# Performance work log

Hardware: AMD Instinct MI355X
Metric: run time of the kernel (lower is better)

## Reference

```python
import jax, jax.numpy as jnp
import numpy as np

ROPE_BASE = 10000.0
NEG_INF = -1e9


def _rope_tables(L, dh, dtype):
    # standard RoPE: inv_freq over half dims, tables shaped [L, dh]
    half = dh // 2
    inv_freq = 1.0 / (ROPE_BASE ** (jnp.arange(0, half, dtype=jnp.float32) * 2.0 / dh))
    freqs = jnp.arange(L, dtype=jnp.float32)[:, None] * inv_freq[None, :]  # [L, half]
    emb = jnp.concatenate([freqs, freqs], axis=-1)  # [L, dh]
    return jnp.cos(emb).astype(dtype), jnp.sin(emb).astype(dtype)


def _apply_rope(t, cos, sin):
    # t: [B, H, L, dh]; rotate-half convention
    dh = t.shape[-1]
    t1, t2 = t[..., : dh // 2], t[..., dh // 2:]
    rot = jnp.concatenate([-t2, t1], axis=-1)
    return t * cos[None, None] + rot * sin[None, None]


def setup_inputs() -> dict:
    key = jax.random.key(0)
    ks = jax.random.split(key, 7)
    B, L, D, nh = 2, 2048, 2048, 16
    s = 0.02
    return {
        "x": jax.random.normal(ks[0], (B, L, D), dtype=jnp.float32),
        "Wq": jax.random.normal(ks[1], (D, 2 * D), dtype=jnp.float32) * s,
        "Wk": jax.random.normal(ks[2], (D, D), dtype=jnp.float32) * s,
        "Wv": jax.random.normal(ks[3], (D, D), dtype=jnp.float32) * s,
        "Wl": jax.random.normal(ks[4], (D, nh), dtype=jnp.float32) * s,
        "bl": jnp.zeros((nh,), dtype=jnp.float32),
        "Wo": jax.random.normal(ks[5], (D, D), dtype=jnp.float32) * s,
    }


def reference(x, Wq, Wk, Wv, Wl, bl, Wo):
    B, L, D = x.shape
    nh = Wl.shape[1]
    dh = D // nh

    q = (x @ Wq).reshape(B, L, 2 * nh, dh).transpose(0, 2, 1, 3)  # [B, 2nh, L, dh]
    k = (x @ Wk).reshape(B, L, nh, dh).transpose(0, 2, 1, 3)      # [B, nh, L, dh]
    v = (x @ Wv).reshape(B, L, nh, dh).transpose(0, 2, 1, 3)      # [B, nh, L, dh]

    cos, sin = _rope_tables(L, dh, x.dtype)
    q = _apply_rope(q, cos, sin)
    k = _apply_rope(k, cos, sin)

    # pair query heads (2i, 2i+1) share k/v head i — avoid repeat_interleave
    qp = q.reshape(B, nh, 2, L, dh)
    scale = 1.0 / jnp.sqrt(jnp.asarray(dh, dtype=x.dtype))
    scores = jnp.einsum("bhpqd,bhkd->bhpqk", qp, k) * scale  # [B, nh, 2, L, L]
    causal = jnp.tril(jnp.ones((L, L), dtype=bool))
    scores = jnp.where(causal[None, None, None], scores, NEG_INF)
    probs = jax.nn.softmax(scores, axis=-1)
    ctx = jnp.einsum("bhpqk,bhkd->bhpqd", probs, v)  # [B, nh, 2, L, dh]

    lam = jax.nn.sigmoid(x @ Wl + bl).transpose(0, 2, 1)[..., None]  # [B, nh, L, 1]
    out = ctx[:, :, 0] - lam * ctx[:, :, 1]  # [B, nh, L, dh]
    out = out.transpose(0, 2, 1, 3).reshape(B, L, D)
    return out @ Wo
```

## Files before the change

### kernel.cpp

```cpp
#include <hip/hip_runtime.h>
#include <cstddef>
#include <cstdint>

#define L_SEQ 2048
#define D_MODEL 2048
#define NH 16
#define DH 128
#define M_ROWS 4096

__device__ __forceinline__ ushort f2bf(float f) {
    union { __bf16 b; ushort u; } v; v.b = (__bf16)f; return v.u;
}
__device__ __forceinline__ float bf2f(ushort h) {
    union { uint32_t u; float f; } v; v.u = ((uint32_t)h) << 16; return v.f;
}
__device__ __forceinline__ float2 bf2f2(uint32_t u) {
    union { uint32_t u; float f; } lo, hi;
    lo.u = u << 16; hi.u = u & 0xffff0000u;
    return make_float2(lo.f, hi.f);
}

__device__ __forceinline__ void gld_lds16(const void* g, void* l) {
    __builtin_amdgcn_global_load_lds(
        (const __attribute__((address_space(1))) void*)g,
        (__attribute__((address_space(3))) void*)l, 16, 0, 0);
}

typedef __bf16  bf16x8 __attribute__((ext_vector_type(8)));
typedef float   f32x4  __attribute__((ext_vector_type(4)));

__global__ __launch_bounds__(256) void cvt_bf16(
    const float* __restrict__ in, ushort* __restrict__ out)
{
    const int i = (blockIdx.x * 256 + threadIdx.x) * 8;
    const float4 a = *(const float4*)&in[i];
    const float4 b = *(const float4*)&in[i + 4];
    uint4 o;
    o.x = (uint)f2bf(a.x) | ((uint)f2bf(a.y) << 16);
    o.y = (uint)f2bf(a.z) | ((uint)f2bf(a.w) << 16);
    o.z = (uint)f2bf(b.x) | ((uint)f2bf(b.y) << 16);
    o.w = (uint)f2bf(b.z) | ((uint)f2bf(b.w) << 16);
    *(uint4*)&out[i] = o;
}

__global__ __launch_bounds__(256) void transpose_cvt(
    const float* __restrict__ W, ushort* __restrict__ Wt, int K, int N)
{
    __shared__ float tile[32][33];
    const int n0 = blockIdx.x * 32, k0 = blockIdx.y * 32;
    const int t = threadIdx.x;
    const int r = t >> 3;
    const int c4 = (t & 7) * 4;
    const float4 v = *(const float4*)&W[(size_t)(k0 + r) * N + n0 + c4];
    tile[r][c4 + 0] = v.x; tile[r][c4 + 1] = v.y;
    tile[r][c4 + 2] = v.z; tile[r][c4 + 3] = v.w;
    __syncthreads();
    ushort4 o;
    o.x = f2bf(tile[c4 + 0][r]);
    o.y = f2bf(tile[c4 + 1][r]);
    o.z = f2bf(tile[c4 + 2][r]);
    o.w = f2bf(tile[c4 + 3][r]);
    *(ushort4*)&Wt[(size_t)(n0 + r) * K + k0 + c4] = o;
}

__global__ __launch_bounds__(256) void rope_table(float2* __restrict__ tab)
{
    const int i = blockIdx.x * 256 + threadIdx.x;
    const int d = i & 63, l = i >> 6;
    const float inv = exp2f(-(float)d * 0.20762050593045857f);
    const float ang = (float)l * inv;
    float s, c;
    sincosf(ang, &s, &c);
    tab[i] = make_float2(c, s);
}

__global__ __launch_bounds__(256) void rope_k(
    ushort* __restrict__ T, const float2* __restrict__ tab)
{
    const int idx = blockIdx.x * 256 + threadIdx.x;
    const int d2   = (idx & 31) * 2;
    const int head = (idx >> 5) & 15;
    const int row  = idx >> 9;
    const int l    = row & (L_SEQ - 1);
    const size_t base = (size_t)row * 2048 + head * 128 + d2;
    const uint a = *(const uint*)&T[base];
    const uint b = *(const uint*)&T[base + 64];
    const float2 t0 = bf2f2(a);
    const float2 t1 = bf2f2(b);
    const float2 cs0 = tab[l * 64 + d2];
    const float2 cs1 = tab[l * 64 + d2 + 1];
    const float o0x = t0.x * cs0.x - t1.x * cs0.y;
    const float o0y = t0.y * cs1.x - t1.y * cs1.y;
    const float o1x = t1.x * cs0.x + t0.x * cs0.y;
    const float o1y = t1.y * cs1.x + t0.y * cs1.y;
    *(uint*)&T[base]      = (uint)f2bf(o0x) | ((uint)f2bf(o0y) << 16);
    *(uint*)&T[base + 64] = (uint)f2bf(o1x) | ((uint)f2bf(o1y) << 16);
}

template <int MODE>
__global__ __launch_bounds__(256) void gemm_bf16(
    const ushort* __restrict__ A, const ushort* __restrict__ Bt,
    void* __restrict__ Cv, int M, int N, int K)
{
    __shared__ __align__(16) ushort As[128 * 32];
    __shared__ __align__(16) ushort Bs[128 * 32];
    const int bm = blockIdx.y * 128;
    const int bn = blockIdx.x * 128;
    const int t = threadIdx.x;
    const int w = t >> 6, lane = t & 63;
    const int wm = (w & 1) * 64;
    const int wn = (w >> 1) * 64;

    const int srow = t >> 2;
    const int scol = (t & 3) * 8;
    const ushort* Ag  = A  + (size_t)(bm + srow) * K + scol;
    const ushort* Ag2 = A  + (size_t)(bm + 64 + srow) * K + scol;
    const ushort* Bg  = Bt + (size_t)(bn + srow) * K + scol;
    const ushort* Bg2 = Bt + (size_t)(bn + 64 + srow) * K + scol;
    ushort* Asl  = &As[(size_t)t * 8];
    ushort* Asl2 = &As[(size_t)(t + 256) * 8];
    ushort* Bsl  = &Bs[(size_t)t * 8];
    ushort* Bsl2 = &Bs[(size_t)(t + 256) * 8];

    const int fr = lane & 15;
    const int fq = (lane >> 4) * 8;
    const ushort* Abase = &As[(size_t)(wm + fr) * 32 + fq];
    const ushort* Bbase = &Bs[(size_t)(wn + fr) * 32 + fq];

    f32x4 acc[4][4] = {};

    for (int k0 = 0; k0 < K; k0 += 32) {
        __syncthreads();
        gld_lds16(Ag + k0, Asl);
        gld_lds16(Ag2 + k0, Asl2);
        gld_lds16(Bg + k0, Bsl);
        gld_lds16(Bg2 + k0, Bsl2);
        __syncthreads();
        bf16x8 a[4], b[4];
        #pragma unroll
        for (int i = 0; i < 4; ++i) {
            a[i] = *(const bf16x8*)(Abase + (size_t)i * 16 * 32);
            b[i] = *(const bf16x8*)(Bbase + (size_t)i * 16 * 32);
        }
        #pragma unroll
        for (int mt = 0; mt < 4; ++mt)
            #pragma unroll
            for (int nt = 0; nt < 4; ++nt)
                acc[mt][nt] = __builtin_amdgcn_mfma_f32_16x16x32_bf16(
                    a[mt], b[nt], acc[mt][nt], 0, 0, 0);
    }

    const int crow = (lane >> 4) * 4;
    const int ccol = lane & 15;
    #pragma unroll
    for (int mt = 0; mt < 4; ++mt) {
        #pragma unroll
        for (int nt = 0; nt < 4; ++nt) {
            if (MODE == 3) {
                const size_t row = bm + wm + mt * 16 + crow;
                const size_t col = bn + wn + nt * 16 + ccol;
                ushort4 o4;
                o4.x = f2bf(acc[mt][nt][0]); o4.y = f2bf(acc[mt][nt][1]);
                o4.z = f2bf(acc[mt][nt][2]); o4.w = f2bf(acc[mt][nt][3]);
                *(ushort4*)&((ushort*)Cv)[
                    ((row >> 11) * 16 + (col >> 7)) * (size_t)(128 * 2048)
                    + (col & 127) * 2048 + (row & 2047)] = o4;
            } else {
                #pragma unroll
                for (int reg = 0; reg < 4; ++reg) {
                    const size_t row = bm + wm + mt * 16 + crow + reg;
                    const size_t col = bn + wn + nt * 16 + ccol;
                    if (MODE == 1) {
                        ((ushort*)Cv)[row * N + col] = f2bf(acc[mt][nt][reg]);
                    } else {
                        ((float*)Cv)[row * N + col] = acc[mt][nt][reg];
                    }
                }
            }
        }
    }
}

__global__ __launch_bounds__(256) void lam_kernel(
    const float* __restrict__ X, const float* __restrict__ Wl,
    const float* __restrict__ bl, float* __restrict__ Lam)
{
    const int idx  = blockIdx.x * 256 + threadIdx.x;
    const int hh   = idx & 15;
    const int part = (idx >> 4) & 1;
    const int m    = idx >> 5;
    const float* xr = X + (size_t)m * D_MODEL + part * 1024;
    const float* wl = Wl + (size_t)(part * 1024) * NH;
    float acc = 0.0f;
    for (int d = 0; d < 1024; d += 4) {
        const float4 xv = *(const float4*)&xr[d];
        acc += xv.x * wl[(d + 0) * NH + hh];
        acc += xv.y * wl[(d + 1) * NH + hh];
        acc += xv.z * wl[(d + 2) * NH + hh];
        acc += xv.w * wl[(d + 3) * NH + hh];
    }
    acc += __shfl_xor(acc, 16);
    if (part == 0) {
        acc += bl[hh];
        Lam[(size_t)m * NH + hh] = 1.0f / (1.0f + expf(-acc));
    }
}

__global__ __launch_bounds__(256, 2) void attn_mfma(
    const ushort* __restrict__ Qb, const ushort* __restrict__ Kb,
    const ushort* __restrict__ Vtg, const float* __restrict__ Lam,
    const float2* __restrict__ Rtab, ushort* __restrict__ OutB)
{
    __shared__ __align__(16) ushort lds[33792];
    ushort* P_sh = lds + 24576;

    const int h  = blockIdx.y;
    const int b  = blockIdx.z;
    const int pt = blockIdx.x;
    const int t  = threadIdx.x;
    const int w = t >> 6, lane = t & 63;
    const int colL = lane & 15, quad = lane >> 4;
    const int p = w >> 1, slot = w & 1;
    ushort* Pw = P_sh + w * (32 * 72);

    const ushort* Kgbase = Kb  + (size_t)(b * 2048) * 2048 + h * 128;
    const ushort* Vgbase = Vtg + (size_t)((b * 16 + h) * 128) * 2048;
    const float scale2 = 0.12751744f;

    auto stageK = [&](ushort* dst, int kt0) {
        #pragma unroll
        for (int j = 0; j < 4; ++j) {
            const int idx = j * 256 + t;
            const int kr = idx >> 4;
            const int kg = t & 15;
            gld_lds16(Kgbase + (size_t)(kt0 + kr) * 2048 + ((kg ^ (kr & 15)) << 3),
                      dst + (size_t)idx * 8);
        }
    };
    auto stageV = [&](ushort* dst, int kt0) {
        #pragma unroll
        for (int j = 0; j < 4; ++j) {
            const int idx = j * 256 + t;
            const int vr = idx >> 3;
            const int vg = t & 7;
            gld_lds16(Vgbase + (size_t)vr * 2048 + kt0 + ((vg ^ (vr & 7)) << 3),
                      dst + (size_t)idx * 8);
        }
    };

    for (int ph = 0; ph < 2; ++ph) {
        const int qt  = ph ? pt : 31 - pt;
        const int q0  = qt * 64;
        const int r0w = q0 + slot * 32;

        bf16x8 qf[2][4];
        #pragma unroll
        for (int g = 0; g < 2; ++g) {
            const int l = r0w + g * 16 + colL;
            const ushort* Qr = Qb + (size_t)(b * 2048 + l) * 4096
                             + (2 * h + p) * 128 + quad * 8;
            ushort raw[4][8];
            #pragma unroll
            for (int c = 0; c < 4; ++c)
                *(uint4*)raw[c] = *(const uint4*)&Qr[c * 32];
            const float2* tb = Rtab + l * 64 + quad * 8;
            ushort o[4][8];
            #pragma unroll
            for (int c = 0; c < 2; ++c)
                #pragma unroll
                for (int j = 0; j < 8; ++j) {
                    const float2 cs = tb[c * 32 + j];
                    const float a  = bf2f(raw[c][j]);
                    const float bb = bf2f(raw[c + 2][j]);
                    o[c][j]     = f2bf(a * cs.x - bb * cs.y);
                    o[c + 2][j] = f2bf(bb * cs.x + a * cs.y);
                }
            #pragma unroll
            for (int c = 0; c < 4; ++c)
                qf[g][c] = *(const bf16x8*)o[c];
        }

        f32x4 ctx[2][8] = {};
        float m2[2][4] = {{-1e30f,-1e30f,-1e30f,-1e30f},
                          {-1e30f,-1e30f,-1e30f,-1e30f}};
        float li[2][4] = {};

        ushort* Kc = lds;
        ushort* Vc = lds + 8192;
        ushort* Fr = lds + 16384;

        stageK(Kc, 0);
        stageV(Vc, 0);
        __syncthreads();

        for (int kt = 0; kt <= qt; ++kt) {
            const int kt0 = kt * 64;

            f32x4 sc2[2][4] = {};
            __builtin_amdgcn_s_setprio(1);
            #pragma unroll
            for (int c = 0; c < 4; ++c)
                #pragma unroll
                for (int nt = 0; nt < 4; ++nt) {
                    const int krow = nt * 16 + colL;
                    const bf16x8 kf = *(const bf16x8*)
                        &Kc[krow * 128 + (((c * 4 + quad) ^ (krow & 15)) << 3)];
                    sc2[0][nt] = __builtin_amdgcn_mfma_f32_16x16x32_bf16(
                        qf[0][c], kf, sc2[0][nt], 0, 0, 0);
                    sc2[1][nt] = __builtin_amdgcn_mfma_f32_16x16x32_bf16(
                        qf[1][c], kf, sc2[1][nt], 0, 0, 0);
                }
            __builtin_amdgcn_s_setprio(0);

            __syncthreads();
            if (kt < qt) {
                stageK(Fr, kt0 + 64);
                stageV(Kc, kt0 + 64);
            }

            const bool dmask = (kt == qt);
            #pragma unroll
            for (int g = 0; g < 2; ++g)
                #pragma unroll
                for (int reg = 0; reg < 4; ++reg) {
                    const int row = r0w + g * 16 + quad * 4 + reg;
                    float s[4];
                    #pragma unroll
                    for (int nt = 0; nt < 4; ++nt) {
                        float v = sc2[g][nt][reg] * scale2;
                        if (dmask && (kt0 + nt * 16 + colL > row)) v = -1e9f;
                        s[nt] = v;
                    }
                    float mx = fmaxf(fmaxf(s[0], s[1]), fmaxf(s[2], s[3]));
                    #pragma unroll
                    for (int off = 8; off >= 1; off >>= 1)
                        mx = fmaxf(mx, __shfl_xor(mx, off));
                    if (__any(mx > m2[g][reg] + 11.0f)) {
                        const float mnew  = fmaxf(m2[g][reg], mx);
                        const float alpha = exp2f(m2[g][reg] - mnew);
                        li[g][reg] *= alpha;
                        m2[g][reg] = mnew;
                        #pragma unroll
                        for (int nt2 = 0; nt2 < 8; ++nt2)
                            ctx[g][nt2][reg] *= alpha;
                    }
                    float rs = 0.f;
                    #pragma unroll
                    for (int nt = 0; nt < 4; ++nt) {
                        const float pv = exp2f(s[nt] - m2[g][reg]);
                        s[nt] = pv;
                        rs += pv;
                    }
                    #pragma unroll
                    for (int off = 8; off >= 1; off >>= 1)
                        rs += __shfl_xor(rs, off);
                    li[g][reg] += rs;
                    #pragma unroll
                    for (int nt = 0; nt < 4; ++nt)
                        Pw[(g * 16 + quad * 4 + reg) * 72 + nt * 16 + colL]
                            = f2bf(s[nt]);
                }

            __builtin_amdgcn_s_setprio(1);
            #pragma unroll
            for (int c2 = 0; c2 < 2; ++c2) {
                const bf16x8 pf0 = *(const bf16x8*)
                    &Pw[colL * 72 + c2 * 32 + quad * 8];
                const bf16x8 pf1 = *(const bf16x8*)
                    &Pw[(16 + colL) * 72 + c2 * 32 + quad * 8];
                #pragma unroll
                for (int nt2 = 0; nt2 < 8; ++nt2) {
                    const int vrow = nt2 * 16 + colL;
                    const bf16x8 vf = *(const bf16x8*)
                        &Vc[vrow * 64 + (((c2 * 4 + quad) ^ (vrow & 7)) << 3)];
                    ctx[0][nt2] = __builtin_amdgcn_mfma_f32_16x16x32_bf16(
                        pf0, vf, ctx[0][nt2], 0, 0, 0);
                    ctx[1][nt2] = __builtin_amdgcn_mfma_f32_16x16x32_bf16(
                        pf1, vf, ctx[1][nt2], 0, 0, 0);
                }
            }
            __builtin_amdgcn_s_setprio(0);

            __syncthreads();
            ushort* tmp = Fr; Fr = Vc; Vc = Kc; Kc = tmp;
        }

        float invl[2][4];
        #pragma unroll
        for (int g = 0; g < 2; ++g)
            #pragma unroll
            for (int reg = 0; reg < 4; ++reg)
                invl[g][reg] = 1.0f / li[g][reg];

        float* comb = (float*)lds;
        __syncthreads();
        if (p == 1) {
            #pragma unroll
            for (int g = 0; g < 2; ++g)
                #pragma unroll
                for (int nt2 = 0; nt2 < 8; ++nt2)
                    #pragma unroll
                    for (int reg = 0; reg < 4; ++reg)
                        comb[(slot * 32 + g * 16 + quad * 4 + reg) * 130
                             + nt2 * 16 + colL] = ctx[g][nt2][reg] * invl[g][reg];
        }
        __syncthreads();
        if (p == 0) {
            #pragma unroll
            for (int g = 0; g < 2; ++g)
                #pragma unroll
                for (int reg = 0; reg < 4; ++reg) {
                    const int row = r0w + g * 16 + quad * 4 + reg;
                    const float lamv = Lam[(size_t)(b * 2048 + row) * 16 + h];
                    ushort* orow = OutB + (size_t)(b * 2048 + row) * 2048 + h * 128;
                    #pragma unroll
                    for (int nt2 = 0; nt2 < 8; ++nt2) {
                        const float c1 = comb[(slot * 32 + g * 16 + quad * 4 + reg) * 130
                                              + nt2 * 16 + colL];
                        const float o = ctx[g][nt2][reg] * invl[g][reg] - lamv * c1;
                        orow[nt2 * 16 + colL] = f2bf(o);
                    }
                }
        }
        __syncthreads();
    }
}

extern "C" void kernel_launch(void* const* d_in, const int* in_sizes, int n_in,
                              void* d_out, int out_size, void* d_ws, size_t ws_size,
                              hipStream_t stream)
{
    const float* x  = (const float*)d_in[0];
    const float* Wq = (const float*)d_in[1];
    const float* Wk = (const float*)d_in[2];
    const float* Wv = (const float*)d_in[3];
    const float* Wl = (const float*)d_in[4];
    const float* bl = (const float*)d_in[5];
    const float* Wo = (const float*)d_in[6];
    float* out = (float*)d_out;
    (void)ws_size; (void)in_sizes; (void)n_in; (void)out_size;

    ushort* ws   = (ushort*)d_ws;
    ushort* xb   = ws;
    ushort* Qb16 = xb   + (size_t)8388608;
    ushort* Kb16 = Qb16 + (size_t)16777216;
    ushort* Vtg  = Kb16 + (size_t)8388608;
    ushort* Wqt  = Vtg  + (size_t)8388608;
    ushort* Wkt  = Wqt  + (size_t)8388608;
    ushort* Wvt  = Wkt  + (size_t)4194304;
    ushort* Wot  = Wvt  + (size_t)4194304;
    ushort* OutB = Wot  + (size_t)4194304;
    float*  LamB = (float*)(OutB + (size_t)8388608);
    float2* Rtab = (float2*)(LamB + (size_t)65536);

    cvt_bf16<<<4096, 256, 0, stream>>>(x, xb);
    transpose_cvt<<<dim3(128, 64), 256, 0, stream>>>(Wq, Wqt, 2048, 4096);
    transpose_cvt<<<dim3(64, 64), 256, 0, stream>>>(Wk, Wkt, 2048, 2048);
    transpose_cvt<<<dim3(64, 64), 256, 0, stream>>>(Wv, Wvt, 2048, 2048);
    transpose_cvt<<<dim3(64, 64), 256, 0, stream>>>(Wo, Wot, 2048, 2048);
    lam_kernel<<<512, 256, 0, stream>>>(x, Wl, bl, LamB);
    rope_table<<<512, 256, 0, stream>>>(Rtab);

    gemm_bf16<1><<<dim3(32, 32), 256, 0, stream>>>(xb, Wqt, Qb16, M_ROWS, 4096, D_MODEL);
    gemm_bf16<1><<<dim3(16, 32), 256, 0, stream>>>(xb, Wkt, Kb16, M_ROWS, D_MODEL, D_MODEL);
    gemm_bf16<3><<<dim3(16, 32), 256, 0, stream>>>(xb, Wvt, Vtg, M_ROWS, D_MODEL, D_MODEL);

    rope_k<<<8192, 256, 0, stream>>>(Kb16, Rtab);

    attn_mfma<<<dim3(16, NH, 2), 256, 0, stream>>>(Qb16, Kb16, Vtg, LamB, Rtab, OutB);

    gemm_bf16<0><<<dim3(16, 32), 256, 0, stream>>>(OutB, Wot, out, M_ROWS, D_MODEL, D_MODEL);
}
```

Before: 632.7 us.

## Replace 128x128 GEMM with double-buffered 256x256 swizzled-LDS MFMA GEMM

The bf16 GEMM moves from 128x128 tiles with 4 waves and a single LDS buffer (BK=32) to 256x256 tiles with 8 waves, BK=64, XOR-swizzled LDS, and double buffering. The next K-tile is staged during MFMA compute, with interleaved barriers and setprio. The aim is more data reuse per byte loaded, hiding global load latency, and fewer LDS bank conflicts across all four projection GEMMs. In exchange it needs 128KB of LDS and many more accumulator registers per block. The grid also shrinks to 128–256 blocks, which may underfill the CUs.

Measured after the change: 649.0 us. 2.6% more time.

```diff
diff --git a/kernel.cpp b/kernel.cpp
--- a/kernel.cpp
+++ b/kernel.cpp
@@ -98,82 +98,123 @@
 }
 
 template <int MODE>
-__global__ __launch_bounds__(256) void gemm_bf16(
+__global__ __launch_bounds__(512, 2) void gemm256(
     const ushort* __restrict__ A, const ushort* __restrict__ Bt,
     void* __restrict__ Cv, int M, int N, int K)
 {
-    __shared__ __align__(16) ushort As[128 * 32];
-    __shared__ __align__(16) ushort Bs[128 * 32];
-    const int bm = blockIdx.y * 128;
-    const int bn = blockIdx.x * 128;
+    __shared__ __align__(16) ushort lds[65536];
     const int t = threadIdx.x;
-    const int w = t >> 6, lane = t & 63;
-    const int wm = (w & 1) * 64;
-    const int wn = (w >> 1) * 64;
-
-    const int srow = t >> 2;
-    const int scol = (t & 3) * 8;
-    const ushort* Ag  = A  + (size_t)(bm + srow) * K + scol;
-    const ushort* Ag2 = A  + (size_t)(bm + 64 + srow) * K + scol;
-    const ushort* Bg  = Bt + (size_t)(bn + srow) * K + scol;
-    const ushort* Bg2 = Bt + (size_t)(bn + 64 + srow) * K + scol;
-    ushort* Asl  = &As[(size_t)t * 8];
-    ushort* Asl2 = &As[(size_t)(t + 256) * 8];
-    ushort* Bsl  = &Bs[(size_t)t * 8];
-    ushort* Bsl2 = &Bs[(size_t)(t + 256) * 8];
-
+    const int lane = t & 63;
+    const int w = t >> 6;
+    const int wr = w >> 2, wc = w & 3;
+    const int bm = blockIdx.y * 256;
+    const int bn = blockIdx.x * 256;
     const int fr = lane & 15;
-    const int fq = (lane >> 4) * 8;
-    const ushort* Abase = &As[(size_t)(wm + fr) * 32 + fq];
-    const ushort* Bbase = &Bs[(size_t)(wn + fr) * 32 + fq];
-
-    f32x4 acc[4][4] = {};
-
-    for (int k0 = 0; k0 < K; k0 += 32) {
-        __syncthreads();
-        gld_lds16(Ag + k0, Asl);
-        gld_lds16(Ag2 + k0, Asl2);
-        gld_lds16(Bg + k0, Bsl);
-        gld_lds16(Bg2 + k0, Bsl2);
-        __syncthreads();
-        bf16x8 a[4], b[4];
+    const int quad = lane >> 4;
+
+    const int sr0 = t >> 3;
+    const int sg0 = (t & 7) ^ (sr0 & 7);
+
+    const int nkt = K >> 6;
+
+    f32x4 acc[8][4] = {};
+
+    #pragma unroll
+    for (int q = 0; q < 4; ++q) {
+        ushort* dst = &lds[(q < 2 ? q * 8192 : 16384 + (q - 2) * 8192)
+                           + (size_t)t * 8];
+        const ushort* src = (q < 2)
+            ? A  + (size_t)(bm + q * 128 + sr0) * K + sg0 * 8
+            : Bt + (size_t)(bn + (q - 2) * 128 + sr0) * K + sg0 * 8;
+        gld_lds16(src, dst);
+        gld_lds16(src + (size_t)64 * K, dst + 4096);
+    }
+    __syncthreads();
+
+    for (int kt = 0; kt < nkt; ++kt) {
+        const int d = kt & 1;
+        const ushort* Ah = &lds[d * 32768 + wr * 8192];
+        const ushort* Bh = &lds[d * 32768 + 16384 + (wc >> 1) * 8192];
+        const int brow0 = (wc & 1) * 64;
+        const bool doStage = (kt + 1 < nkt);
+        const int ktN = (kt + 1) * 64;
+
         #pragma unroll
-        for (int i = 0; i < 4; ++i) {
-            a[i] = *(const bf16x8*)(Abase + (size_t)i * 16 * 32);
-            b[i] = *(const bf16x8*)(Bbase + (size_t)i * 16 * 32);
-        }
-        #pragma unroll
-        for (int mt = 0; mt < 4; ++mt)
-            #pragma unroll
-            for (int nt = 0; nt < 4; ++nt)
-                acc[mt][nt] = __builtin_amdgcn_mfma_f32_16x16x32_bf16(
-                    a[mt], b[nt], acc[mt][nt], 0, 0, 0);
+        for (int q = 0; q < 4; ++q) {
+            const int mq = q >> 1, nq = q & 1;
+            bf16x8 af[4][2], bfr[2][2];
+            #pragma unroll
+            for (int i = 0; i < 4; ++i)
+                #pragma unroll
+                for (int ks = 0; ks < 2; ++ks) {
+                    const int r = mq * 64 + i * 16 + fr;
+                    const int slot = (quad + ks * 4) ^ (r & 7);
+                    af[i][ks] = *(const bf16x8*)&Ah[r * 64 + slot * 8];
+                }
+            #pragma unroll
+            for (int j = 0; j < 2; ++j)
+                #pragma unroll
+                for (int ks = 0; ks < 2; ++ks) {
+                    const int rb = brow0 + nq * 32 + j * 16 + fr;
+                    const int slot = (quad + ks * 4) ^ (rb & 7);
+                    bfr[j][ks] = *(const bf16x8*)&Bh[rb * 64 + slot * 8];
+                }
+            if (doStage) {
+                ushort* dst = &lds[(d ^ 1) * 32768
+                    + (q < 2 ? q * 8192 : 16384 + (q - 2) * 8192)
+                    + (size_t)t * 8];
+                const ushort* src = (q < 2)
+                    ? A  + (size_t)(bm + q * 128 + sr0) * K + ktN + sg0 * 8
+                    : Bt + (size_t)(bn + (q - 2) * 128 + sr0) * K + ktN + sg0 * 8;
+                gld_lds16(src, dst);
+                gld_lds16(src + (size_t)64 * K, dst + 4096);
+            }
+            __builtin_amdgcn_s_barrier();
+            asm volatile("s_waitcnt lgkmcnt(0)" ::: "memory");
+            __builtin_amdgcn_sched_barrier(0);
+            __builtin_amdgcn_s_setprio(1);
+            #pragma unroll
+            for (int i = 0; i < 4; ++i)
+                #pragma unroll
+                for (int j = 0; j < 2; ++j)
+                    #pragma unroll
+                    for (int ks = 0; ks < 2; ++ks)
+                        acc[mq * 4 + i][nq * 2 + j] =
+                            __builtin_amdgcn_mfma_f32_16x16x32_bf16(
+                                af[i][ks], bfr[j][ks],
+                                acc[mq * 4 + i][nq * 2 + j], 0, 0, 0);
+            __builtin_amdgcn_s_setprio(0);
+            if (q == 3)
+                asm volatile("s_waitcnt vmcnt(0)" ::: "memory");
+            __builtin_amdgcn_s_barrier();
+            __builtin_amdgcn_sched_barrier(0);
+        }
     }
 
     const int crow = (lane >> 4) * 4;
     const int ccol = lane & 15;
     #pragma unroll
-    for (int mt = 0; mt < 4; ++mt) {
+    for (int mf = 0; mf < 8; ++mf) {
         #pragma unroll
-        for (int nt = 0; nt < 4; ++nt) {
+        for (int nf = 0; nf < 4; ++nf) {
             if (MODE == 3) {
-                const size_t row = bm + wm + mt * 16 + crow;
-                const size_t col = bn + wn + nt * 16 + ccol;
+                const size_t row = bm + wr * 128 + mf * 16 + crow;
+                const size_t col = bn + wc * 64 + nf * 16 + ccol;
                 ushort4 o4;
-                o4.x = f2bf(acc[mt][nt][0]); o4.y = f2bf(acc[mt][nt][1]);
-                o4.z = f2bf(acc[mt][nt][2]); o4.w = f2bf(acc[mt][nt][3]);
+                o4.x = f2bf(acc[mf][nf][0]); o4.y = f2bf(acc[mf][nf][1]);
+                o4.z = f2bf(acc[mf][nf][2]); o4.w = f2bf(acc[mf][nf][3]);
                 *(ushort4*)&((ushort*)Cv)[
                     ((row >> 11) * 16 + (col >> 7)) * (size_t)(128 * 2048)
                     + (col & 127) * 2048 + (row & 2047)] = o4;
             } else {
                 #pragma unroll
                 for (int reg = 0; reg < 4; ++reg) {
-                    const size_t row = bm + wm + mt * 16 + crow + reg;
-                    const size_t col = bn + wn + nt * 16 + ccol;
+                    const size_t row = bm + wr * 128 + mf * 16 + crow + reg;
+                    const size_t col = bn + wc * 64 + nf * 16 + ccol;
                     if (MODE == 1) {
-                        ((ushort*)Cv)[row * N + col] = f2bf(acc[mt][nt][reg]);
+                        ((ushort*)Cv)[row * N + col] = f2bf(acc[mf][nf][reg]);
                     } else {
-                        ((float*)Cv)[row * N + col] = acc[mt][nt][reg];
+                        ((float*)Cv)[row * N + col] = acc[mf][nf][reg];
                     }
                 }
             }
@@ -461,13 +502,13 @@
     lam_kernel<<<512, 256, 0, stream>>>(x, Wl, bl, LamB);
     rope_table<<<512, 256, 0, stream>>>(Rtab);
 
-    gemm_bf16<1><<<dim3(32, 32), 256, 0, stream>>>(xb, Wqt, Qb16, M_ROWS, 4096, D_MODEL);
-    gemm_bf16<1><<<dim3(16, 32), 256, 0, stream>>>(xb, Wkt, Kb16, M_ROWS, D_MODEL, D_MODEL);
-    gemm_bf16<3><<<dim3(16, 32), 256, 0, stream>>>(xb, Wvt, Vtg, M_ROWS, D_MODEL, D_MODEL);
+    gemm256<1><<<dim3(16, 16), 512, 0, stream>>>(xb, Wqt, Qb16, M_ROWS, 4096, D_MODEL);
+    gemm256<1><<<dim3(8, 16), 512, 0, stream>>>(xb, Wkt, Kb16, M_ROWS, D_MODEL, D_MODEL);
+    gemm256<3><<<dim3(8, 16), 512, 0, stream>>>(xb, Wvt, Vtg, M_ROWS, D_MODEL, D_MODEL);
 
     rope_k<<<8192, 256, 0, stream>>>(Kb16, Rtab);
 
     attn_mfma<<<dim3(16, NH, 2), 256, 0, stream>>>(Qb16, Kb16, Vtg, LamB, Rtab, OutB);
 
-    gemm_bf16<0><<<dim3(16, 32), 256, 0, stream>>>(OutB, Wot, out, M_ROWS, D_MODEL, D_MODEL);
-}
+    gemm256<0><<<dim3(8, 16), 512, 0, stream>>>(OutB, Wot, out, M_ROWS, D_MODEL, D_MODEL);
+}
```
